# Kernel tuning notes

Measured on AMD Instinct MI355X. Metric: run time of the kernel, lower is better.

Reference implementation:

```python
import jax, jax.numpy as jnp
import numpy as np

N_NODES = 50000
N_EDGES = 800000
IN_FEATS = 128
OUT_FEATS = 128


def setup_inputs() -> dict:
    key = jax.random.key(0)
    k_feat, k_src, k_dst, k_w1, k_w2, k_lw = jax.random.split(key, 6)
    feat = jax.random.normal(k_feat, (N_NODES, IN_FEATS), dtype=jnp.float32)
    src_idx = jax.random.randint(k_src, (N_EDGES,), 0, N_NODES, dtype=jnp.int64 if jax.config.jax_enable_x64 else jnp.int32)
    dst_idx = jax.random.randint(k_dst, (N_EDGES,), 0, N_NODES, dtype=jnp.int64 if jax.config.jax_enable_x64 else jnp.int32)
    # xavier-uniform-ish scales
    w1_lim = float(np.sqrt(6.0 / (2 * IN_FEATS + IN_FEATS)))
    w2_lim = float(np.sqrt(6.0 / (IN_FEATS + OUT_FEATS)))
    lw_lim = float(np.sqrt(2.0) * np.sqrt(6.0 / (IN_FEATS + OUT_FEATS)))
    weight1 = jax.random.uniform(k_w1, (2 * IN_FEATS, IN_FEATS), jnp.float32, -w1_lim, w1_lim)
    weight2 = jax.random.uniform(k_w2, (IN_FEATS, OUT_FEATS), jnp.float32, -w2_lim, w2_lim)
    loop_weight = jax.random.uniform(k_lw, (IN_FEATS, OUT_FEATS), jnp.float32, -lw_lim, lw_lim)
    bias = jnp.zeros((OUT_FEATS,), dtype=jnp.float32)
    return {
        "feat": feat,
        "src_idx": src_idx,
        "dst_idx": dst_idx,
        "weight1": weight1,
        "weight2": weight2,
        "loop_weight": loop_weight,
        "bias": bias,
    }


def reference(feat, src_idx, dst_idx, weight1, weight2, loop_weight, bias):
    # Gather per-edge src/dst features and concat: [E, 2*d]
    feat_msg = jnp.concatenate([feat[src_idx], feat[dst_idx]], axis=-1)
    # 2-layer edge MLP: relu(msg @ W1) @ W2 -> [E, out]
    e_msg = jnp.matmul(jax.nn.relu(jnp.matmul(feat_msg, weight1)), weight2)
    # Scatter-sum to destination nodes: [N, out]
    rst = jax.ops.segment_sum(e_msg, dst_idx, num_segments=feat.shape[0])
    # bias + residual loop message
    rst = rst + bias + jnp.matmul(feat, loop_weight)
    return rst
```

## Files before the change

### kernel.cpp

```cpp
#include <hip/hip_runtime.h>

typedef __attribute__((ext_vector_type(8))) unsigned short ushort8v;
typedef __attribute__((ext_vector_type(8))) short short8v;
typedef __attribute__((ext_vector_type(4))) float f32x4;

#define CAP 64
#define BINSTRIDE 2560

__device__ inline unsigned short f2bf(float f) {
    union { float f; unsigned u; } v; v.f = f;
    unsigned u = v.u;
    unsigned r = (u + 0x7FFFu + ((u >> 16) & 1u)) >> 16;
    return (unsigned short)r;
}
__device__ inline float bf2f(unsigned short h) {
    union { unsigned u; float f; } v; v.u = ((unsigned)h) << 16;
    return v.f;
}
__device__ inline unsigned pkbf(float lo, float hi) {
    unsigned r;
    asm("v_cvt_pk_bf16_f32 %0, %1, %2" : "=v"(r) : "v"(lo), "v"(hi));
    return r;
}

__global__ __launch_bounds__(256) void prep_weights(
    const float* __restrict__ W1, const float* __restrict__ W2,
    const float* __restrict__ LW,
    unsigned short* __restrict__ W1t, unsigned short* __restrict__ W3t) {
    int i = blockIdx.x * 256 + threadIdx.x;
    if (i < 32768) {
        int jj = i >> 7, k = i & 127;
        float v = (jj < 128) ? W1[k * 128 + jj] : W1[(128 + k) * 128 + (jj - 128)];
        W1t[i] = f2bf(v);
    } else {
        int i2 = i - 32768;
        int n = i2 >> 8, k = i2 & 255;
        float v = (k < 128) ? W2[k * 128 + n] : LW[(k - 128) * 128 + n];
        W3t[i2] = f2bf(v);
    }
}

__global__ __launch_bounds__(256) void bin_edges(
    const int* __restrict__ src, const int* __restrict__ dst,
    int* __restrict__ binCur, unsigned* __restrict__ binPairs,
    int E, int NBINS) {
    __shared__ int hist[512];
    __shared__ int bse[512];
    int tid = threadIdx.x;
    for (int j = tid; j < NBINS; j += 256) hist[j] = 0;

    int s[16], d[16];
    int base = blockIdx.x * 4096;
#pragma unroll
    for (int i = 0; i < 4; i++) {
        int e = base + i * 1024 + tid * 4;
        if (e + 3 < E) {
            int4 dv = *(const int4*)(dst + e);
            int4 sv = *(const int4*)(src + e);
            d[i * 4 + 0] = dv.x; d[i * 4 + 1] = dv.y;
            d[i * 4 + 2] = dv.z; d[i * 4 + 3] = dv.w;
            s[i * 4 + 0] = sv.x; s[i * 4 + 1] = sv.y;
            s[i * 4 + 2] = sv.z; s[i * 4 + 3] = sv.w;
        } else {
#pragma unroll
            for (int k = 0; k < 4; k++) {
                int ee = e + k;
                if (ee < E) { d[i * 4 + k] = dst[ee]; s[i * 4 + k] = src[ee]; }
                else d[i * 4 + k] = -1;
            }
        }
    }
    __syncthreads();
#pragma unroll
    for (int k = 0; k < 16; k++)
        if (d[k] >= 0) atomicAdd(&hist[d[k] >> 7], 1);
    __syncthreads();
    for (int j = tid; j < NBINS; j += 256) {
        int c = hist[j];
        bse[j] = c ? atomicAdd(&binCur[j], c) : 0;
        hist[j] = 0;
    }
    __syncthreads();
#pragma unroll
    for (int k = 0; k < 16; k++) {
        if (d[k] < 0) continue;
        int b = d[k] >> 7;
        int p = bse[b] + atomicAdd(&hist[b], 1);
        if (p < BINSTRIDE)
            binPairs[(size_t)b * BINSTRIDE + p] =
                ((unsigned)(d[k] & 127) << 16) | (unsigned)s[k];
    }
}

__global__ __launch_bounds__(256) void build_buckets(
    const int* __restrict__ binCur, const unsigned* __restrict__ binPairs,
    int* __restrict__ cur, unsigned short* __restrict__ eSrc,
    int N, int NBINS) {
    __shared__ unsigned pairs[BINSTRIDE];
    __shared__ int deg[128], rnk[128];
    int b = blockIdx.x, tid = threadIdx.x;
    if (b >= NBINS) return;
    int cnt = min(binCur[b], BINSTRIDE);
    if (tid < 128) { deg[tid] = 0; rnk[tid] = 0; }
    __syncthreads();
    for (int i = tid; i < cnt; i += 256) {
        unsigned pr = binPairs[(size_t)b * BINSTRIDE + i];
        pairs[i] = pr;
        atomicAdd(&deg[pr >> 16], 1);
    }
    __syncthreads();
    int node0 = b << 7;
    if (tid < 128 && node0 + tid < N) cur[node0 + tid] = deg[tid];
    for (int i = tid; i < cnt; i += 256) {
        unsigned pr = pairs[i];
        int dl = pr >> 16;
        int pos = atomicAdd(&rnk[dl], 1);
        if (pos < CAP)
            eSrc[(size_t)(node0 + dl) * CAP + pos] = (unsigned short)(pr & 0xFFFF);
    }
}

template <int BK, int AMODE, bool OUT_BF16>
__device__ void gemm_tile(
    unsigned short* As, unsigned short* Bs,
    const unsigned short* __restrict__ Abf, int lda,
    const float* __restrict__ Af32,
    const unsigned short* __restrict__ Bt, int ldb, int nRowsB,
    void* __restrict__ Cout, int ldc,
    const float* __restrict__ bias, int M, int K, int m0, int n0) {
    const int tid = threadIdx.x;
    const int lane = tid & 63;
    const int w = tid >> 6;
    const int wr = w >> 1, wc = w & 1;
    const int q = lane >> 4, ln = lane & 15;
    const int BPR = BK / 8;
    const int ITERS = BK / 16;

    f32x4 acc[4][4];
#pragma unroll
    for (int i = 0; i < 4; i++)
#pragma unroll
        for (int j = 0; j < 4; j++) acc[i][j] = (f32x4)0.f;

    for (int kk = 0; kk < K; kk += BK) {
        const bool aF32 = (AMODE == 1) || (AMODE == 2 && kk >= 128);
#pragma unroll
        for (int i = 0; i < ITERS; i++) {
            int id = i * 256 + tid;
            int r = id / BPR, bb = id % BPR;
            int gr = m0 + r;
            unsigned short* dstp = As + r * BK + ((bb ^ (r & (BPR - 1))) * 8);
            if (aF32) {
                float4 lo = make_float4(0.f, 0.f, 0.f, 0.f), hi = lo;
                if (gr < M) {
                    const float* p = Af32 + (size_t)gr * 128 +
                                     (AMODE == 2 ? kk - 128 : kk) + bb * 8;
                    lo = *(const float4*)p;
                    hi = *(const float4*)(p + 4);
                }
                *(uint4*)dstp = make_uint4(pkbf(lo.x, lo.y), pkbf(lo.z, lo.w),
                                           pkbf(hi.x, hi.y), pkbf(hi.z, hi.w));
            } else {
                ushort8v v = (ushort8v)(unsigned short)0;
                if (gr < M) v = *(const ushort8v*)(Abf + (size_t)gr * lda + kk + bb * 8);
                *(ushort8v*)dstp = v;
            }
        }
#pragma unroll
        for (int i = 0; i < ITERS; i++) {
            int id = i * 256 + tid;
            int r = id / BPR, bb = id % BPR;
            ushort8v v = (ushort8v)(unsigned short)0;
            int gr = n0 + r;
            if (gr < nRowsB) v = *(const ushort8v*)(Bt + (size_t)gr * ldb + kk + bb * 8);
            *(ushort8v*)(Bs + r * BK + ((bb ^ (r & (BPR - 1))) * 8)) = v;
        }
        __syncthreads();
#pragma unroll
        for (int ks = 0; ks < BK / 32; ks++) {
            short8v af[4], bfv[4];
#pragma unroll
            for (int ti = 0; ti < 4; ti++) {
                int m = wr * 64 + ti * 16 + ln;
                int blk = (ks * 4 + q) ^ (m & (BPR - 1));
                af[ti] = *(const short8v*)(As + m * BK + blk * 8);
            }
#pragma unroll
            for (int tj = 0; tj < 4; tj++) {
                int n = wc * 64 + tj * 16 + ln;
                int blk = (ks * 4 + q) ^ (n & (BPR - 1));
                bfv[tj] = *(const short8v*)(Bs + n * BK + blk * 8);
            }
#pragma unroll
            for (int ti = 0; ti < 4; ti++)
#pragma unroll
                for (int tj = 0; tj < 4; tj++)
                    acc[ti][tj] = __builtin_amdgcn_mfma_f32_16x16x32_bf16(
                        af[ti], bfv[tj], acc[ti][tj], 0, 0, 0);
        }
        if (kk + BK < K) __syncthreads();
    }

#pragma unroll
    for (int ti = 0; ti < 4; ti++) {
        int rowb = m0 + wr * 64 + ti * 16 + q * 4;
#pragma unroll
        for (int tj = 0; tj < 4; tj++) {
            int col = n0 + wc * 64 + tj * 16 + ln;
            f32x4 c = acc[ti][tj];
            float bv = 0.f;
            if (!OUT_BF16 && bias) bv = bias[col];
#pragma unroll
            for (int r = 0; r < 4; r++) {
                int row = rowb + r;
                if (row < M) {
                    if (OUT_BF16)
                        ((unsigned short*)Cout)[(size_t)row * ldc + col] = f2bf(c[r]);
                    else
                        ((float*)Cout)[(size_t)row * ldc + col] = c[r] + bv;
                }
            }
        }
    }
}

__global__ __launch_bounds__(256) void gemm1_kernel(
    const float* __restrict__ feat, const unsigned short* __restrict__ W1t,
    unsigned short* __restrict__ AB, int N) {
    __shared__ unsigned short smem[2 * 128 * 128];
    gemm_tile<128, 1, true>(smem, smem + 128 * 128, nullptr, 0, feat, W1t, 128, 256,
                            (void*)AB, 256, nullptr, N, 128,
                            blockIdx.x * 128, blockIdx.y * 128);
}

__global__ __launch_bounds__(256) void gemm2_kernel(
    const unsigned short* __restrict__ S2, const float* __restrict__ feat,
    const unsigned short* __restrict__ W3t,
    float* __restrict__ out, const float* __restrict__ bias, int M) {
    __shared__ unsigned short smem[2 * 128 * 128];
    gemm_tile<128, 2, false>(smem, smem + 128 * 128, S2, 128, feat, W3t, 256, 128,
                             (void*)out, 128, bias, M, 256, blockIdx.x * 128, 0);
}

__global__ __launch_bounds__(256) void gather_kernel(
    const unsigned short* __restrict__ AB, const int* __restrict__ cur,
    const unsigned short* __restrict__ eSrc,
    unsigned short* __restrict__ S2, int N) {
    int wid = (blockIdx.x * 256 + threadIdx.x) >> 6;
    int lane = threadIdx.x & 63;
    if (wid >= N) return;
    int num = min(cur[wid], CAP);
    size_t start = (size_t)wid * CAP;
    int half = lane >> 5, ln32 = lane & 31;
    ushort4 bv = *(const ushort4*)(AB + (size_t)wid * 256 + 128 + ln32 * 4);
    float b0 = bf2f(bv.x), b1 = bf2f(bv.y), b2 = bf2f(bv.z), b3 = bf2f(bv.w);
    float p0 = 0.f, p1 = 0.f, p2 = 0.f, p3 = 0.f;

    int mySrc = (lane < num) ? (int)eSrc[start + lane] : 0;
    int j = 0;
    for (; j + 16 <= num; j += 16) {
        ushort4 v[8];
#pragma unroll
        for (int u = 0; u < 8; u++) {
            int s = __shfl(mySrc, j + 2 * u + half);
            v[u] = *(const ushort4*)(AB + (size_t)s * 256 + ln32 * 4);
        }
#pragma unroll
        for (int u = 0; u < 8; u++) {
            p0 += fmaxf(bf2f(v[u].x) + b0, 0.f);
            p1 += fmaxf(bf2f(v[u].y) + b1, 0.f);
            p2 += fmaxf(bf2f(v[u].z) + b2, 0.f);
            p3 += fmaxf(bf2f(v[u].w) + b3, 0.f);
        }
    }
    for (; j + 4 <= num; j += 4) {
        ushort4 v[2];
#pragma unroll
        for (int u = 0; u < 2; u++) {
            int s = __shfl(mySrc, j + 2 * u + half);
            v[u] = *(const ushort4*)(AB + (size_t)s * 256 + ln32 * 4);
        }
#pragma unroll
        for (int u = 0; u < 2; u++) {
            p0 += fmaxf(bf2f(v[u].x) + b0, 0.f);
            p1 += fmaxf(bf2f(v[u].y) + b1, 0.f);
            p2 += fmaxf(bf2f(v[u].z) + b2, 0.f);
            p3 += fmaxf(bf2f(v[u].w) + b3, 0.f);
        }
    }
    for (; j < num; j += 2) {
        int idx = j + half;
        int s = __shfl(mySrc, idx);
        bool ok = idx < num;
        ushort4 v = *(const ushort4*)(AB + (size_t)s * 256 + ln32 * 4);
        float m = ok ? 1.f : 0.f;
        p0 += m * fmaxf(bf2f(v.x) + b0, 0.f);
        p1 += m * fmaxf(bf2f(v.y) + b1, 0.f);
        p2 += m * fmaxf(bf2f(v.z) + b2, 0.f);
        p3 += m * fmaxf(bf2f(v.w) + b3, 0.f);
    }
    p0 += __shfl_xor(p0, 32);
    p1 += __shfl_xor(p1, 32);
    p2 += __shfl_xor(p2, 32);
    p3 += __shfl_xor(p3, 32);
    if (half == 0) {
        *(ushort4*)(S2 + (size_t)wid * 128 + ln32 * 4) =
            make_ushort4(f2bf(p0), f2bf(p1), f2bf(p2), f2bf(p3));
    }
}

extern "C" void kernel_launch(void* const* d_in, const int* in_sizes, int n_in,
                              void* d_out, int out_size, void* d_ws, size_t ws_size,
                              hipStream_t stream) {
    const float* feat = (const float*)d_in[0];
    const int* src = (const int*)d_in[1];
    const int* dst = (const int*)d_in[2];
    const float* W1 = (const float*)d_in[3];
    const float* W2 = (const float*)d_in[4];
    const float* LW = (const float*)d_in[5];
    const float* bias = (const float*)d_in[6];
    float* out = (float*)d_out;

    const int N = in_sizes[0] / 128;
    const int E = in_sizes[1];
    const int NBINS = (N + 127) / 128;

    char* ws = (char*)d_ws;
    unsigned short* S2 = (unsigned short*)ws;
    size_t off = (size_t)N * 128 * 2;
    unsigned short* AB = (unsigned short*)(ws + off);
    off += (size_t)N * 256 * 2;
    unsigned short* W1t = (unsigned short*)(ws + off);
    off += (size_t)256 * 128 * 2;
    unsigned short* W3t = (unsigned short*)(ws + off);
    off += (size_t)128 * 256 * 2;
    int* cur = (int*)(ws + off);
    off += (size_t)N * 4;
    unsigned short* eSrc = (unsigned short*)(ws + off);
    off += (size_t)N * CAP * 2;
    int* binCur = (int*)(ws + off);
    off += (size_t)NBINS * 4;
    unsigned* binPairs = (unsigned*)(ws + off);
    off += (size_t)NBINS * BINSTRIDE * 4;

    hipMemsetAsync(binCur, 0, (size_t)NBINS * 4, stream);
    prep_weights<<<256, 256, 0, stream>>>(W1, W2, LW, W1t, W3t);

    bin_edges<<<(E + 4095) / 4096, 256, 0, stream>>>(
        src, dst, binCur, binPairs, E, NBINS);
    build_buckets<<<NBINS, 256, 0, stream>>>(binCur, binPairs, cur, eSrc, N, NBINS);

    dim3 g1((N + 127) / 128, 2);
    gemm1_kernel<<<g1, 256, 0, stream>>>(feat, W1t, AB, N);

    gather_kernel<<<(N + 3) / 4, 256, 0, stream>>>(AB, cur, eSrc, S2, N);

    gemm2_kernel<<<(N + 127) / 128, 256, 0, stream>>>(S2, feat, W3t, out, bias, N);
}
```

Measured before the change: 179.1 us.

## Fuse edge binning into gemm1 launch and fold binCur memset into prep

Merges the edge-binning kernel and the first feature GEMM into one launch, with even blocks computing a 128x256 output tile and odd blocks binning 2048-edge chunks, so the two independent stages can run side by side. The binCur zeroing moves into prep_weights, which removes a memset launch. The gemm1 tile now covers all 256 output columns with K-chunks of 64 and XOR-swizzled LDS, and gemm2 uses a smaller K-tile of 64 to cut shared memory. This raises register pressure through the 4x8 accumulator array and gives blocks in one launch uneven amounts of work.

```diff
diff --git a/kernel.cpp b/kernel.cpp
--- a/kernel.cpp
+++ b/kernel.cpp
@@ -26,8 +26,12 @@
 __global__ __launch_bounds__(256) void prep_weights(
     const float* __restrict__ W1, const float* __restrict__ W2,
     const float* __restrict__ LW,
-    unsigned short* __restrict__ W1t, unsigned short* __restrict__ W3t) {
-    int i = blockIdx.x * 256 + threadIdx.x;
+    unsigned short* __restrict__ W1t, unsigned short* __restrict__ W3t,
+    int* __restrict__ binCur, int NBINS) {
+    int tid = threadIdx.x;
+    if (blockIdx.x == 0)
+        for (int j = tid; j < NBINS; j += 256) binCur[j] = 0;
+    int i = blockIdx.x * 256 + tid;
     if (i < 32768) {
         int jj = i >> 7, k = i & 127;
         float v = (jj < 128) ? W1[k * 128 + jj] : W1[(128 + k) * 128 + (jj - 128)];
@@ -40,55 +44,140 @@
     }
 }
 
-__global__ __launch_bounds__(256) void bin_edges(
+__global__ __launch_bounds__(256) void gemm1_bin(
+    const float* __restrict__ feat, const unsigned short* __restrict__ W1t,
+    unsigned short* __restrict__ AB,
     const int* __restrict__ src, const int* __restrict__ dst,
     int* __restrict__ binCur, unsigned* __restrict__ binPairs,
-    int E, int NBINS) {
-    __shared__ int hist[512];
-    __shared__ int bse[512];
-    int tid = threadIdx.x;
-    for (int j = tid; j < NBINS; j += 256) hist[j] = 0;
-
-    int s[16], d[16];
-    int base = blockIdx.x * 4096;
-#pragma unroll
-    for (int i = 0; i < 4; i++) {
-        int e = base + i * 1024 + tid * 4;
-        if (e + 3 < E) {
-            int4 dv = *(const int4*)(dst + e);
-            int4 sv = *(const int4*)(src + e);
-            d[i * 4 + 0] = dv.x; d[i * 4 + 1] = dv.y;
-            d[i * 4 + 2] = dv.z; d[i * 4 + 3] = dv.w;
-            s[i * 4 + 0] = sv.x; s[i * 4 + 1] = sv.y;
-            s[i * 4 + 2] = sv.z; s[i * 4 + 3] = sv.w;
+    int E, int NC, int NT, int M, int NBINS) {
+    __shared__ unsigned short smem[(128 + 256) * 64];
+    const int tid = threadIdx.x;
+    const int bid = blockIdx.x;
+
+    if ((bid & 1) == 0) {
+        int tile = bid >> 1;
+        if (tile >= NT) return;
+        int m0 = tile * 128;
+        const int lane = tid & 63, w = tid >> 6;
+        const int wr = w >> 1, wc = w & 1;
+        const int q = lane >> 4, ln = lane & 15;
+        unsigned short* As = smem;
+        unsigned short* Bs = smem + 128 * 64;
+
+        f32x4 acc[4][8];
+#pragma unroll
+        for (int i = 0; i < 4; i++)
+#pragma unroll
+            for (int j = 0; j < 8; j++) acc[i][j] = (f32x4)0.f;
+
+        for (int kk = 0; kk < 128; kk += 64) {
+#pragma unroll
+            for (int i = 0; i < 4; i++) {
+                int id = i * 256 + tid;
+                int r = id >> 3, bb = id & 7, gr = m0 + r;
+                unsigned short* dstp = As + r * 64 + ((bb ^ (r & 7)) * 8);
+                float4 lo = make_float4(0.f, 0.f, 0.f, 0.f), hi = lo;
+                if (gr < M) {
+                    const float* p = feat + (size_t)gr * 128 + kk + bb * 8;
+                    lo = *(const float4*)p;
+                    hi = *(const float4*)(p + 4);
+                }
+                *(uint4*)dstp = make_uint4(pkbf(lo.x, lo.y), pkbf(lo.z, lo.w),
+                                           pkbf(hi.x, hi.y), pkbf(hi.z, hi.w));
+            }
+#pragma unroll
+            for (int i = 0; i < 8; i++) {
+                int id = i * 256 + tid;
+                int r = id >> 3, bb = id & 7;
+                ushort8v v = *(const ushort8v*)(W1t + (size_t)r * 128 + kk + bb * 8);
+                *(ushort8v*)(Bs + r * 64 + ((bb ^ (r & 7)) * 8)) = v;
+            }
+            __syncthreads();
+#pragma unroll
+            for (int ks = 0; ks < 2; ks++) {
+                short8v af[4], bv[8];
+#pragma unroll
+                for (int ti = 0; ti < 4; ti++) {
+                    int m = wr * 64 + ti * 16 + ln;
+                    int blk = (ks * 4 + q) ^ (m & 7);
+                    af[ti] = *(const short8v*)(As + m * 64 + blk * 8);
+                }
+#pragma unroll
+                for (int tj = 0; tj < 8; tj++) {
+                    int n = wc * 128 + tj * 16 + ln;
+                    int blk = (ks * 4 + q) ^ (n & 7);
+                    bv[tj] = *(const short8v*)(Bs + n * 64 + blk * 8);
+                }
+#pragma unroll
+                for (int ti = 0; ti < 4; ti++)
+#pragma unroll
+                    for (int tj = 0; tj < 8; tj++)
+                        acc[ti][tj] = __builtin_amdgcn_mfma_f32_16x16x32_bf16(
+                            af[ti], bv[tj], acc[ti][tj], 0, 0, 0);
+            }
+            if (kk == 0) __syncthreads();
+        }
+#pragma unroll
+        for (int ti = 0; ti < 4; ti++) {
+            int rowb = m0 + wr * 64 + ti * 16 + q * 4;
+#pragma unroll
+            for (int tj = 0; tj < 8; tj++) {
+                int col = wc * 128 + tj * 16 + ln;
+                f32x4 c = acc[ti][tj];
+#pragma unroll
+                for (int r = 0; r < 4; r++) {
+                    int row = rowb + r;
+                    if (row < M)
+                        AB[(size_t)row * 256 + col] = f2bf(c[r]);
+                }
+            }
+        }
+    } else {
+        int chunk = bid >> 1;
+        if (chunk >= NC) return;
+        int* hist = (int*)smem;
+        int* bse = hist + 512;
+        for (int j = tid; j < NBINS; j += 256) hist[j] = 0;
+
+        int s[8], d[8];
+        int base = chunk * 2048 + tid * 8;
+        if (base + 7 < E) {
+            int4 s0 = *(const int4*)(src + base);
+            int4 s1 = *(const int4*)(src + base + 4);
+            int4 d0 = *(const int4*)(dst + base);
+            int4 d1 = *(const int4*)(dst + base + 4);
+            s[0] = s0.x; s[1] = s0.y; s[2] = s0.z; s[3] = s0.w;
+            s[4] = s1.x; s[5] = s1.y; s[6] = s1.z; s[7] = s1.w;
+            d[0] = d0.x; d[1] = d0.y; d[2] = d0.z; d[3] = d0.w;
+            d[4] = d1.x; d[5] = d1.y; d[6] = d1.z; d[7] = d1.w;
         } else {
 #pragma unroll
-            for (int k = 0; k < 4; k++) {
-                int ee = e + k;
-                if (ee < E) { d[i * 4 + k] = dst[ee]; s[i * 4 + k] = src[ee]; }
-                else d[i * 4 + k] = -1;
-            }
-        }
-    }
-    __syncthreads();
-#pragma unroll
-    for (int k = 0; k < 16; k++)
-        if (d[k] >= 0) atomicAdd(&hist[d[k] >> 7], 1);
-    __syncthreads();
-    for (int j = tid; j < NBINS; j += 256) {
-        int c = hist[j];
-        bse[j] = c ? atomicAdd(&binCur[j], c) : 0;
-        hist[j] = 0;
-    }
-    __syncthreads();
-#pragma unroll
-    for (int k = 0; k < 16; k++) {
-        if (d[k] < 0) continue;
-        int b = d[k] >> 7;
-        int p = bse[b] + atomicAdd(&hist[b], 1);
-        if (p < BINSTRIDE)
-            binPairs[(size_t)b * BINSTRIDE + p] =
-                ((unsigned)(d[k] & 127) << 16) | (unsigned)s[k];
+            for (int k = 0; k < 8; k++) {
+                int ee = base + k;
+                if (ee < E) { d[k] = dst[ee]; s[k] = src[ee]; }
+                else d[k] = -1;
+            }
+        }
+        __syncthreads();
+#pragma unroll
+        for (int k = 0; k < 8; k++)
+            if (d[k] >= 0) atomicAdd(&hist[d[k] >> 7], 1);
+        __syncthreads();
+        for (int j = tid; j < NBINS; j += 256) {
+            int c = hist[j];
+            bse[j] = c ? atomicAdd(&binCur[j], c) : 0;
+            hist[j] = 0;
+        }
+        __syncthreads();
+#pragma unroll
+        for (int k = 0; k < 8; k++) {
+            if (d[k] < 0) continue;
+            int b = d[k] >> 7;
+            int p = bse[b] + atomicAdd(&hist[b], 1);
+            if (p < BINSTRIDE)
+                binPairs[(size_t)b * BINSTRIDE + p] =
+                    ((unsigned)(d[k] & 127) << 16) | (unsigned)s[k];
+        }
     }
 }
 
@@ -224,22 +313,13 @@
     }
 }
 
-__global__ __launch_bounds__(256) void gemm1_kernel(
-    const float* __restrict__ feat, const unsigned short* __restrict__ W1t,
-    unsigned short* __restrict__ AB, int N) {
-    __shared__ unsigned short smem[2 * 128 * 128];
-    gemm_tile<128, 1, true>(smem, smem + 128 * 128, nullptr, 0, feat, W1t, 128, 256,
-                            (void*)AB, 256, nullptr, N, 128,
-                            blockIdx.x * 128, blockIdx.y * 128);
-}
-
 __global__ __launch_bounds__(256) void gemm2_kernel(
     const unsigned short* __restrict__ S2, const float* __restrict__ feat,
     const unsigned short* __restrict__ W3t,
     float* __restrict__ out, const float* __restrict__ bias, int M) {
-    __shared__ unsigned short smem[2 * 128 * 128];
-    gemm_tile<128, 2, false>(smem, smem + 128 * 128, S2, 128, feat, W3t, 256, 128,
-                             (void*)out, 128, bias, M, 256, blockIdx.x * 128, 0);
+    __shared__ unsigned short smem[2 * 128 * 64];
+    gemm_tile<64, 2, false>(smem, smem + 128 * 64, S2, 128, feat, W3t, 256, 128,
+                            (void*)out, 128, bias, M, 256, blockIdx.x * 128, 0);
 }
 
 __global__ __launch_bounds__(256) void gather_kernel(
@@ -343,16 +423,16 @@
     unsigned* binPairs = (unsigned*)(ws + off);
     off += (size_t)NBINS * BINSTRIDE * 4;
 
-    hipMemsetAsync(binCur, 0, (size_t)NBINS * 4, stream);
-    prep_weights<<<256, 256, 0, stream>>>(W1, W2, LW, W1t, W3t);
-
-    bin_edges<<<(E + 4095) / 4096, 256, 0, stream>>>(
-        src, dst, binCur, binPairs, E, NBINS);
+    prep_weights<<<256, 256, 0, stream>>>(W1, W2, LW, W1t, W3t, binCur, NBINS);
+
+    int NT = (N + 127) / 128;
+    int NC = (E + 2047) / 2048;
+    int mx = NT > NC ? NT : NC;
+    gemm1_bin<<<2 * mx, 256, 0, stream>>>(
+        feat, W1t, AB, src, dst, binCur, binPairs, E, NC, NT, N, NBINS);
+
     build_buckets<<<NBINS, 256, 0, stream>>>(binCur, binPairs, cur, eSrc, N, NBINS);
 
-    dim3 g1((N + 127) / 128, 2);
-    gemm1_kernel<<<g1, 256, 0, stream>>>(feat, W1t, AB, N);
-
     gather_kernel<<<(N + 3) / 4, 256, 0, stream>>>(AB, cur, eSrc, S2, N);
 
     gemm2_kernel<<<(N + 127) / 128, 256, 0, stream>>>(S2, feat, W3t, out, bias, N);
```

After: 182.1 us. Within noise of the previous version (+1.7%).
